# Kernel tuning notes

Measured on AMD Instinct MI355X. Metric: run time of the kernel, lower is better.

## Reference

```python
import jax, jax.numpy as jnp
import numpy as np

N = 32768       # total nodes = NUM_GRAPHS * T
F_IN = 32       # num_features
HC = 64         # hidden_channels
HEADS = 4
E = 524288      # edges before self-loops
NUM_GRAPHS = 64 # == batch.max()+1 by construction
T = 512         # time steps per graph (N // NUM_GRAPHS)
OUT = 24        # output_size
NEG_SLOPE = 0.2 # PyG GATConv default


def gat_layer(x, src, dst, W, a_src, a_dst, b, n_nodes):
    """PyG GATConv (concat=True) with edge softmax over incoming edges."""
    H, C = a_src.shape
    h = (x @ W).reshape(n_nodes, H, C)                    # [N,H,C]
    alpha_src = jnp.sum(h * a_src, axis=-1)               # [N,H]
    alpha_dst = jnp.sum(h * a_dst, axis=-1)               # [N,H]
    e = jax.nn.leaky_relu(alpha_src[src] + alpha_dst[dst], NEG_SLOPE)  # [E,H]
    m = jax.ops.segment_max(e, dst, num_segments=n_nodes)
    e = jnp.exp(e - m[dst])
    s = jax.ops.segment_sum(e, dst, num_segments=n_nodes)
    alpha = e / (s[dst] + 1e-16)                          # [E,H]
    msg = h[src] * alpha[..., None]                       # [E,H,C]
    out = jax.ops.segment_sum(msg, dst, num_segments=n_nodes)  # [N,H,C]
    return out.reshape(n_nodes, H * C) + b


def gru_layer(x, Wih, Whh, bih, bhh):
    """torch nn.GRU single layer, batch_first input x: [B,T,Hin] -> ([B,T,H], h_T)."""
    Bsz = x.shape[0]
    H = Whh.shape[1]

    def step(h, xt):
        gi = xt @ Wih.T + bih
        gh = h @ Whh.T + bhh
        ir, iz, inn = jnp.split(gi, 3, axis=-1)
        hr, hz, hn = jnp.split(gh, 3, axis=-1)
        r = jax.nn.sigmoid(ir + hr)
        z = jax.nn.sigmoid(iz + hz)
        n = jnp.tanh(inn + r * hn)
        h_new = (1.0 - z) * n + z * h
        return h_new, h_new

    h0 = jnp.zeros((Bsz, H), x.dtype)
    hT, ys = jax.lax.scan(step, h0, jnp.swapaxes(x, 0, 1))
    return jnp.swapaxes(ys, 0, 1), hT


def setup_inputs() -> dict:
    key = jax.random.key(0)
    ks = jax.random.split(key, 24)
    sc = 0.1
    inp = {
        "x": jax.random.normal(ks[0], (N, F_IN), dtype=jnp.float32),
        "edge_index": jax.random.randint(ks[1], (2, E), 0, N, dtype=jnp.int32),
        "batch": jnp.repeat(jnp.arange(NUM_GRAPHS, dtype=jnp.int32), T),
        # GAT layer 1: F_IN -> HC x HEADS (concat)
        "W1": sc * jax.random.normal(ks[2], (F_IN, HEADS * HC), dtype=jnp.float32),
        "a_src1": sc * jax.random.normal(ks[3], (HEADS, HC), dtype=jnp.float32),
        "a_dst1": sc * jax.random.normal(ks[4], (HEADS, HC), dtype=jnp.float32),
        "b1": jnp.zeros((HEADS * HC,), dtype=jnp.float32),
        # GAT layer 2: HEADS*HC -> HC, 1 head
        "W2": sc * jax.random.normal(ks[5], (HEADS * HC, HC), dtype=jnp.float32),
        "a_src2": sc * jax.random.normal(ks[6], (1, HC), dtype=jnp.float32),
        "a_dst2": sc * jax.random.normal(ks[7], (1, HC), dtype=jnp.float32),
        "b2": jnp.zeros((HC,), dtype=jnp.float32),
        # GRU (2 layers, input_size == hidden_size == HC)
        "gru_Wih0": sc * jax.random.normal(ks[8], (3 * HC, HC), dtype=jnp.float32),
        "gru_Whh0": sc * jax.random.normal(ks[9], (3 * HC, HC), dtype=jnp.float32),
        "gru_bih0": jnp.zeros((3 * HC,), dtype=jnp.float32),
        "gru_bhh0": jnp.zeros((3 * HC,), dtype=jnp.float32),
        "gru_Wih1": sc * jax.random.normal(ks[10], (3 * HC, HC), dtype=jnp.float32),
        "gru_Whh1": sc * jax.random.normal(ks[11], (3 * HC, HC), dtype=jnp.float32),
        "gru_bih1": jnp.zeros((3 * HC,), dtype=jnp.float32),
        "gru_bhh1": jnp.zeros((3 * HC,), dtype=jnp.float32),
        # Linear head
        "Wl": sc * jax.random.normal(ks[12], (OUT, HC), dtype=jnp.float32),
        "bl": jnp.zeros((OUT,), dtype=jnp.float32),
    }
    return inp


def reference(x, edge_index, batch, W1, a_src1, a_dst1, b1, W2, a_src2, a_dst2, b2,
              gru_Wih0, gru_Whh0, gru_bih0, gru_bhh0,
              gru_Wih1, gru_Whh1, gru_bih1, gru_bhh1, Wl, bl):
    # PyG GATConv default add_self_loops=True
    loops = jnp.arange(N, dtype=edge_index.dtype)
    src = jnp.concatenate([edge_index[0], loops])
    dst = jnp.concatenate([edge_index[1], loops])

    h = jax.nn.elu(gat_layer(x, src, dst, W1, a_src1, a_dst1, b1, N))   # [N, HEADS*HC]
    h = jax.nn.elu(gat_layer(h, src, dst, W2, a_src2, a_dst2, b2, N))   # [N, HC]

    # batch is repeat(arange(NUM_GRAPHS), T) so batch.max()+1 == NUM_GRAPHS (static)
    seq = h.reshape(NUM_GRAPHS, T, HC)
    seq, _ = gru_layer(seq, gru_Wih0, gru_Whh0, gru_bih0, gru_bhh0)
    _, hT = gru_layer(seq, gru_Wih1, gru_Whh1, gru_bih1, gru_bhh1)      # [B, HC]
    return hT @ Wl.T + bl                                               # [B, OUT]
```

## Files before the change

### kernel.cpp

```cpp
#include <hip/hip_runtime.h>
#include <hip/hip_bf16.h>

#define N_NODES 32768
#define F_IN    32
#define HC      64
#define HEADS   4
#define NE      524288
#define NET     (NE + N_NODES)
#define NG      64
#define TT      512
#define OUTF    24

__device__ __forceinline__ float lrelu(float x){ return x > 0.f ? x : 0.2f*x; }
__device__ __forceinline__ float eluf (float x){ return x > 0.f ? x : __expf(x)-1.f; }
__device__ __forceinline__ float sigmf(float x){ return 1.f/(1.f+__expf(-x)); }
__device__ __forceinline__ float tanhfast(float x){ return 1.f - 2.f/(__expf(2.f*x)+1.f); }
__device__ __forceinline__ float bcast(float v, int k){
  return __int_as_float(__builtin_amdgcn_readlane(__float_as_int(v), k));
}

__global__ __launch_bounds__(256) void k_deg(const int* __restrict__ ei,
                                             int* __restrict__ deg){
  int e = blockIdx.x*256 + threadIdx.x;
  int d = (e < NE) ? ei[NE+e] : (e - NE);
  atomicAdd(deg + d, 1);
}

__global__ __launch_bounds__(1024) void k_scan(const int* __restrict__ deg,
                                               int* __restrict__ rowptr){
  __shared__ int ps[1024];
  const int t = threadIdx.x;
  const int base = t*32;
  int local[32]; int s = 0;
  #pragma unroll
  for(int i=0;i<32;i++){ local[i]=deg[base+i]; s+=local[i]; }
  ps[t]=s; __syncthreads();
  for(int off=1; off<1024; off<<=1){
    int v = (t>=off) ? ps[t-off] : 0;
    __syncthreads();
    ps[t]+=v;
    __syncthreads();
  }
  int run = (t==0) ? 0 : ps[t-1];
  #pragma unroll
  for(int i=0;i<32;i++){ rowptr[base+i]=run; run+=local[i]; }
  if(t==1023) rowptr[N_NODES]=run;
}

__global__ __launch_bounds__(256) void k_fill(const int* __restrict__ ei,
                                              const int* __restrict__ rowptr,
                                              int* __restrict__ cur,
                                              int* __restrict__ col){
  int e = blockIdx.x*256 + threadIdx.x;
  int s, d;
  if(e < NE){ s = ei[e]; d = ei[NE+e]; } else { s = e-NE; d = s; }
  int pos = atomicAdd(cur + d, 1);
  col[rowptr[d] + pos] = s;
}

__global__ __launch_bounds__(256) void k_gemm1(const float* __restrict__ x,
                                               const float* __restrict__ W1,
                                               float* __restrict__ h1){
  __shared__ __align__(16) float xs[64*32];
  __shared__ __align__(16) float ws[32*256];
  const int tid = threadIdx.x;
  const int row0 = blockIdx.x*64;
  const float4* xg = (const float4*)(x + row0*F_IN);
  float4* xs4 = (float4*)xs;
  for(int i=tid;i<512;i+=256) xs4[i]=xg[i];
  const float4* wg=(const float4*)W1; float4* ws4=(float4*)ws;
  for(int i=tid;i<2048;i+=256) ws4[i]=wg[i];
  __syncthreads();
  float wc[32];
  #pragma unroll
  for(int k=0;k<32;k++) wc[k]=ws[k*256+tid];
  for(int r=0;r<64;r++){
    const float4* xr=(const float4*)(xs + r*32);
    float acc=0.f;
    #pragma unroll
    for(int k4=0;k4<8;k4++){
      float4 v=xr[k4];
      acc += v.x*wc[4*k4]+v.y*wc[4*k4+1]+v.z*wc[4*k4+2]+v.w*wc[4*k4+3];
    }
    h1[(row0+r)*256+tid]=acc;
  }
}

__global__ __launch_bounds__(256) void k_alpha1(const float* __restrict__ h1,
                                                const float* __restrict__ a_src,
                                                const float* __restrict__ a_dst,
                                                float* __restrict__ as1,
                                                float* __restrict__ ad1){
  int t = blockIdx.x*256 + threadIdx.x;
  int n = t>>2, h = t&3;
  const float4* hp=(const float4*)(h1 + n*256 + h*64);
  const float4* ap=(const float4*)(a_src + h*64);
  const float4* dp=(const float4*)(a_dst + h*64);
  float sa=0.f, sd=0.f;
  #pragma unroll
  for(int i=0;i<16;i++){
    float4 v=hp[i], a=ap[i], d=dp[i];
    sa += v.x*a.x+v.y*a.y+v.z*a.z+v.w*a.w;
    sd += v.x*d.x+v.y*d.y+v.z*d.z+v.w*d.w;
  }
  as1[t]=sa; ad1[t]=sd;
}

__global__ __launch_bounds__(256) void k_gat1(const int* __restrict__ rowptr,
                                              const int* __restrict__ col,
                                              const float* __restrict__ as1,
                                              const float* __restrict__ ad1,
                                              const float* __restrict__ h1,
                                              const float* __restrict__ b1,
                                              float* __restrict__ out1){
  const int node = blockIdx.x*4 + (threadIdx.x>>6);
  const int lane = threadIdx.x & 63;
  const int h    = lane>>4;
  const int beg = rowptr[node], end = rowptr[node+1];
  const float ad = ad1[node*4+h];
  float4 acc = make_float4(0.f,0.f,0.f,0.f);
  float s = 0.f;
  int j = beg;
  for(; j+1 < end; j += 2){
    int s0 = col[j], s1 = col[j+1];
    float w0 = __expf(lrelu(as1[s0*4+h] + ad));
    float w1 = __expf(lrelu(as1[s1*4+h] + ad));
    float4 v0 = *(const float4*)(h1 + s0*256 + lane*4);
    float4 v1 = *(const float4*)(h1 + s1*256 + lane*4);
    acc.x += w0*v0.x + w1*v1.x;
    acc.y += w0*v0.y + w1*v1.y;
    acc.z += w0*v0.z + w1*v1.z;
    acc.w += w0*v0.w + w1*v1.w;
    s += w0 + w1;
  }
  if(j < end){
    int s0 = col[j];
    float w0 = __expf(lrelu(as1[s0*4+h] + ad));
    float4 v0 = *(const float4*)(h1 + s0*256 + lane*4);
    acc.x += w0*v0.x; acc.y += w0*v0.y; acc.z += w0*v0.z; acc.w += w0*v0.w;
    s += w0;
  }
  const float inv = 1.f/(s + 1e-16f);
  float4 bb = ((const float4*)b1)[lane];
  float4 o;
  o.x = eluf(acc.x*inv + bb.x);
  o.y = eluf(acc.y*inv + bb.y);
  o.z = eluf(acc.z*inv + bb.z);
  o.w = eluf(acc.w*inv + bb.w);
  ((float4*)(out1 + node*256))[lane] = o;
}

__global__ __launch_bounds__(256) void k_gemm2(const float* __restrict__ in,
                                               const float* __restrict__ W2,
                                               float* __restrict__ h2){
  __shared__ __align__(16) float xs[64*256];
  const int tid=threadIdx.x;
  const int row0=blockIdx.x*64;
  const float4* xg=(const float4*)(in + row0*256);
  float4* xs4=(float4*)xs;
  for(int i=tid;i<4096;i+=256) xs4[i]=xg[i];
  __syncthreads();
  const int c0=(tid&15)*4;
  const int r0=(tid>>4)*4;
  float acc[4][4]={};
  for(int k=0;k<256;k+=4){
    float wv[4][4];
    #pragma unroll
    for(int i=0;i<4;i++){
      float4 w=*(const float4*)(W2+(k+i)*64+c0);
      wv[i][0]=w.x; wv[i][1]=w.y; wv[i][2]=w.z; wv[i][3]=w.w;
    }
    #pragma unroll
    for(int i=0;i<4;i++){
      float4 xv=*(const float4*)(xs+(r0+i)*256+k);
      #pragma unroll
      for(int j=0;j<4;j++)
        acc[i][j]+=xv.x*wv[0][j]+xv.y*wv[1][j]+xv.z*wv[2][j]+xv.w*wv[3][j];
    }
  }
  #pragma unroll
  for(int i=0;i<4;i++)
    *(float4*)(h2+(row0+r0+i)*64+c0)=make_float4(acc[i][0],acc[i][1],acc[i][2],acc[i][3]);
}

__global__ __launch_bounds__(256) void k_alpha2(const float* __restrict__ h2,
                                                const float* __restrict__ a_src,
                                                const float* __restrict__ a_dst,
                                                float* __restrict__ as2,
                                                float* __restrict__ ad2){
  int n = blockIdx.x*256 + threadIdx.x;
  const float4* hp=(const float4*)(h2+n*64);
  float sa=0.f, sd=0.f;
  #pragma unroll
  for(int i=0;i<16;i++){
    float4 v=hp[i];
    float4 a=((const float4*)a_src)[i];
    float4 d=((const float4*)a_dst)[i];
    sa+=v.x*a.x+v.y*a.y+v.z*a.z+v.w*a.w;
    sd+=v.x*d.x+v.y*d.y+v.z*d.z+v.w*d.w;
  }
  as2[n]=sa; ad2[n]=sd;
}

__global__ __launch_bounds__(256) void k_gat2(const int* __restrict__ rowptr,
                                              const int* __restrict__ col,
                                              const float* __restrict__ as2,
                                              const float* __restrict__ ad2,
                                              const float* __restrict__ h2,
                                              const float* __restrict__ b2,
                                              float* __restrict__ out2){
  const int node = blockIdx.x*4 + (threadIdx.x>>6);
  const int lane = threadIdx.x & 63;
  const int beg = rowptr[node], end = rowptr[node+1];
  const float ad = ad2[node];
  float acc = 0.f, s = 0.f;
  int j = beg;
  for(; j+1 < end; j += 2){
    int s0 = col[j], s1 = col[j+1];
    float w0 = __expf(lrelu(as2[s0] + ad));
    float w1 = __expf(lrelu(as2[s1] + ad));
    acc += w0*h2[s0*64+lane] + w1*h2[s1*64+lane];
    s += w0 + w1;
  }
  if(j < end){
    int s0 = col[j];
    float w0 = __expf(lrelu(as2[s0] + ad));
    acc += w0*h2[s0*64+lane];
    s += w0;
  }
  const float inv = 1.f/(s + 1e-16f);
  out2[node*64+lane] = eluf(acc*inv + b2[lane]);
}

__global__ __launch_bounds__(256) void k_gemm_gi(const float* __restrict__ in,
                                                 const float* __restrict__ Wih,
                                                 const float* __restrict__ bih,
                                                 float* __restrict__ gi){
  __shared__ __align__(16) float xs[64*64];
  __shared__ float wT[64*192];
  const int tid=threadIdx.x;
  const int row0=blockIdx.x*64;
  const float4* xg=(const float4*)(in+row0*64);
  float4* xs4=(float4*)xs;
  for(int i=tid;i<1024;i+=256) xs4[i]=xg[i];
  for(int i=tid;i<12288;i+=256){ wT[(i&63)*192+(i>>6)] = Wih[i]; }
  __syncthreads();
  if(tid<192){
    float wr[64];
    #pragma unroll
    for(int k=0;k<64;k++) wr[k]=wT[k*192+tid];
    const float bj=bih[tid];
    for(int r=0;r<64;r++){
      float acc=bj;
      const float4* xr=(const float4*)(xs+r*64);
      #pragma unroll
      for(int k4=0;k4<16;k4++){
        float4 v=xr[k4];
        acc+=v.x*wr[4*k4]+v.y*wr[4*k4+1]+v.z*wr[4*k4+2]+v.w*wr[4*k4+3];
      }
      gi[(row0+r)*192+tid]=acc;
    }
  }
}

__global__ __launch_bounds__(576,3) void k_gruR(const float* __restrict__ gi1,
                                                const float* __restrict__ Whh0,
                                                const float* __restrict__ bhh0,
                                                const float* __restrict__ Wih1,
                                                const float* __restrict__ bih1,
                                                const float* __restrict__ Whh1,
                                                const float* __restrict__ bhh1,
                                                const float* __restrict__ Wl,
                                                const float* __restrict__ bl,
                                                float* __restrict__ fout){
  __shared__ float h1s[64];
  __shared__ float h2s[64];
  __shared__ float gh1s[192];
  __shared__ float gi2s[192];
  __shared__ float gh2s[192];
  __shared__ float g1r[2][192];
  const int tid  = threadIdx.x;
  const int w    = tid >> 6;
  const int lane = tid & 63;
  const int b    = blockIdx.x;
  const float* gib = gi1 + (size_t)b*TT*192;

  const int crew = w/3;
  const int row  = (w%3)*64 + lane;
  const float* W  = (crew==0) ? Whh0 : (crew==1) ? Wih1 : Whh1;
  const float* bb = (crew==0) ? bhh0 : (crew==1) ? bih1 : bhh1;
  float* dst      = (crew==0) ? gh1s : (crew==1) ? gi2s : gh2s;

  const float4* wp = (const float4*)(W + row*64);
  float4 Wv0=wp[0],  Wv1=wp[1],  Wv2=wp[2],  Wv3=wp[3];
  float4 Wv4=wp[4],  Wv5=wp[5],  Wv6=wp[6],  Wv7=wp[7];
  float4 Wv8=wp[8],  Wv9=wp[9],  WvA=wp[10], WvB=wp[11];
  float4 WvC=wp[12], WvD=wp[13], WvE=wp[14], WvF=wp[15];
  const float bias = bb[row];

  float giv = 0.f;
  if(w < 3){
    g1r[0][row] = gib[row];
    giv = gib[192 + row];
  }
  if(tid < 64){ h1s[tid]=0.f; h2s[tid]=0.f; }
  __syncthreads();

  for(int i=0;i<=TT;i++){
    float hv = (crew==2) ? h2s[lane] : h1s[lane];
    if(w < 3){
      int pst = i+1;
      if(pst < TT) g1r[pst&1][row] = giv;
      int nst = i+2;
      if(nst < TT) giv = gib[nst*192 + row];
    }
    float a0=bias, a1=0.f, a2=0.f, a3=0.f;
#define DOT4(WV, BASE) \
    a0 = fmaf(bcast(hv, BASE+0), WV.x, a0); \
    a1 = fmaf(bcast(hv, BASE+1), WV.y, a1); \
    a2 = fmaf(bcast(hv, BASE+2), WV.z, a2); \
    a3 = fmaf(bcast(hv, BASE+3), WV.w, a3);
    DOT4(Wv0, 0)  DOT4(Wv1, 4)  DOT4(Wv2, 8)  DOT4(Wv3, 12)
    DOT4(Wv4, 16) DOT4(Wv5, 20) DOT4(Wv6, 24) DOT4(Wv7, 28)
    DOT4(Wv8, 32) DOT4(Wv9, 36) DOT4(WvA, 40) DOT4(WvB, 44)
    DOT4(WvC, 48) DOT4(WvD, 52) DOT4(WvE, 56) DOT4(WvF, 60)
#undef DOT4
    dst[row] = (a0+a1)+(a2+a3);
    __syncthreads();
    if(w == 0){
      if(i < TT){
        float r = sigmf(g1r[i&1][lane]     + gh1s[lane]);
        float z = sigmf(g1r[i&1][64+lane]  + gh1s[64+lane]);
        float n = tanhfast(g1r[i&1][128+lane] + r*gh1s[128+lane]);
        h1s[lane] = (1.f-z)*n + z*h1s[lane];
      }
    } else if(w == 3){
      if(i >= 1){
        float r = sigmf(gi2s[lane]     + gh2s[lane]);
        float z = sigmf(gi2s[64+lane]  + gh2s[64+lane]);
        float n = tanhfast(gi2s[128+lane] + r*gh2s[128+lane]);
        h2s[lane] = (1.f-z)*n + z*h2s[lane];
      }
    }
    __syncthreads();
  }

  if(tid < 24){
    float acc = bl[tid];
    const float4* wl4 = (const float4*)(Wl + tid*64);
    #pragma unroll
    for(int k4=0;k4<16;k4++){
      float4 h4 = *(const float4*)(h2s + 4*k4);
      float4 w4 = wl4[k4];
      acc += h4.x*w4.x + h4.y*w4.y + h4.z*w4.z + h4.w*w4.w;
    }
    fout[b*24+tid] = acc;
  }
}

extern "C" void kernel_launch(void* const* d_in, const int* in_sizes, int n_in,
                              void* d_out, int out_size, void* d_ws, size_t ws_size,
                              hipStream_t stream){
  const float* x     =(const float*)d_in[0];
  const int*   ei    =(const int*  )d_in[1];
  const float* W1    =(const float*)d_in[3];
  const float* a_src1=(const float*)d_in[4];
  const float* a_dst1=(const float*)d_in[5];
  const float* b1    =(const float*)d_in[6];
  const float* W2    =(const float*)d_in[7];
  const float* a_src2=(const float*)d_in[8];
  const float* a_dst2=(const float*)d_in[9];
  const float* b2    =(const float*)d_in[10];
  const float* Wih0  =(const float*)d_in[11];
  const float* Whh0  =(const float*)d_in[12];
  const float* bih0  =(const float*)d_in[13];
  const float* bhh0  =(const float*)d_in[14];
  const float* Wih1  =(const float*)d_in[15];
  const float* Whh1  =(const float*)d_in[16];
  const float* bih1  =(const float*)d_in[17];
  const float* bhh1  =(const float*)d_in[18];
  const float* Wl    =(const float*)d_in[19];
  const float* bl    =(const float*)d_in[20];

  float* ws   = (float*)d_ws;
  float* h1   = ws;
  float* gi   = ws;
  float* out1 = ws + 8388608;
  float* out2 = out1;
  float* h2   = ws + 16777216;
  float* as1  = ws + 18874368;
  float* ad1  = as1 + 131072;
  float* as2  = ad1 + 131072;
  float* ad2  = as2 + 32768;
  int* rowptr = (int*)(ad2 + 32768);
  int* deg    = rowptr + 32800;
  int* cur    = deg + 32768;
  int* col    = cur + 32768;
  float* fo   = (float*)d_out;

  hipMemsetAsync(deg, 0, 2*32768*sizeof(int), stream);

  k_deg  <<<2176,256,0,stream>>>(ei,deg);
  k_scan <<<1  ,1024,0,stream>>>(deg,rowptr);
  k_fill <<<2176,256,0,stream>>>(ei,rowptr,cur,col);

  k_gemm1 <<<512 ,256,0,stream>>>(x,W1,h1);
  k_alpha1<<<512 ,256,0,stream>>>(h1,a_src1,a_dst1,as1,ad1);
  k_gat1  <<<8192,256,0,stream>>>(rowptr,col,as1,ad1,h1,b1,out1);
  k_gemm2 <<<512 ,256,0,stream>>>(out1,W2,h2);
  k_alpha2<<<128 ,256,0,stream>>>(h2,a_src2,a_dst2,as2,ad2);
  k_gat2  <<<8192,256,0,stream>>>(rowptr,col,as2,ad2,h2,b2,out2);
  k_gemm_gi<<<512,256,0,stream>>>(out2,Wih0,bih0,gi);
  k_gruR  <<<64 ,576,0,stream>>>(gi,Whh0,bhh0,Wih1,bih1,Whh1,bhh1,Wl,bl,fo);
  (void)in_sizes; (void)n_in; (void)out_size; (void)ws_size;
}
```

Measured before the change: 819.4 us.

## Stage GRU input gates in 64-step LDS chunks instead of per-step prefetch

The recurrent GRU kernel now bulk-loads 64 timesteps of precomputed layer-0 input gates (48KB) into shared memory with float4 copies once per chunk. This replaces the per-step register prefetch and double-buffered LDS writes, taking the global load latency off the serial critical path. Weight registers are pinned with empty asm so they stay in VGPRs, and the launch-bounds occupancy hint drops to 1. In exchange, each chunk boundary adds a bulk-load stall plus a barrier, and the kernel uses much more LDS.

```diff
diff --git a/kernel.cpp b/kernel.cpp
--- a/kernel.cpp
+++ b/kernel.cpp
@@ -263,7 +263,7 @@
   }
 }
 
-__global__ __launch_bounds__(576,3) void k_gruR(const float* __restrict__ gi1,
+__global__ __launch_bounds__(576,1) void k_gruC(const float* __restrict__ gi1,
                                                 const float* __restrict__ Whh0,
                                                 const float* __restrict__ bhh0,
                                                 const float* __restrict__ Wih1,
@@ -278,7 +278,7 @@
   __shared__ float gh1s[192];
   __shared__ float gi2s[192];
   __shared__ float gh2s[192];
-  __shared__ float g1r[2][192];
+  __shared__ __align__(16) float gic[64*192];
   const int tid  = threadIdx.x;
   const int w    = tid >> 6;
   const int lane = tid & 63;
@@ -296,54 +296,68 @@
   float4 Wv4=wp[4],  Wv5=wp[5],  Wv6=wp[6],  Wv7=wp[7];
   float4 Wv8=wp[8],  Wv9=wp[9],  WvA=wp[10], WvB=wp[11];
   float4 WvC=wp[12], WvD=wp[13], WvE=wp[14], WvF=wp[15];
+#define PIN4(V) asm volatile("" : "+v"(V.x), "+v"(V.y), "+v"(V.z), "+v"(V.w))
+  PIN4(Wv0); PIN4(Wv1); PIN4(Wv2); PIN4(Wv3);
+  PIN4(Wv4); PIN4(Wv5); PIN4(Wv6); PIN4(Wv7);
+  PIN4(Wv8); PIN4(Wv9); PIN4(WvA); PIN4(WvB);
+  PIN4(WvC); PIN4(WvD); PIN4(WvE); PIN4(WvF);
+#undef PIN4
   const float bias = bb[row];
 
-  float giv = 0.f;
-  if(w < 3){
-    g1r[0][row] = gib[row];
-    giv = gib[192 + row];
-  }
   if(tid < 64){ h1s[tid]=0.f; h2s[tid]=0.f; }
   __syncthreads();
 
-  for(int i=0;i<=TT;i++){
-    float hv = (crew==2) ? h2s[lane] : h1s[lane];
-    if(w < 3){
-      int pst = i+1;
-      if(pst < TT) g1r[pst&1][row] = giv;
-      int nst = i+2;
-      if(nst < TT) giv = gib[nst*192 + row];
-    }
-    float a0=bias, a1=0.f, a2=0.f, a3=0.f;
 #define DOT4(WV, BASE) \
     a0 = fmaf(bcast(hv, BASE+0), WV.x, a0); \
     a1 = fmaf(bcast(hv, BASE+1), WV.y, a1); \
     a2 = fmaf(bcast(hv, BASE+2), WV.z, a2); \
     a3 = fmaf(bcast(hv, BASE+3), WV.w, a3);
-    DOT4(Wv0, 0)  DOT4(Wv1, 4)  DOT4(Wv2, 8)  DOT4(Wv3, 12)
-    DOT4(Wv4, 16) DOT4(Wv5, 20) DOT4(Wv6, 24) DOT4(Wv7, 28)
-    DOT4(Wv8, 32) DOT4(Wv9, 36) DOT4(WvA, 40) DOT4(WvB, 44)
-    DOT4(WvC, 48) DOT4(WvD, 52) DOT4(WvE, 56) DOT4(WvF, 60)
+#define MATVEC() do{ \
+    float hv = (crew==2) ? h2s[lane] : h1s[lane]; \
+    float a0=bias, a1=0.f, a2=0.f, a3=0.f; \
+    DOT4(Wv0, 0)  DOT4(Wv1, 4)  DOT4(Wv2, 8)  DOT4(Wv3, 12) \
+    DOT4(Wv4, 16) DOT4(Wv5, 20) DOT4(Wv6, 24) DOT4(Wv7, 28) \
+    DOT4(Wv8, 32) DOT4(Wv9, 36) DOT4(WvA, 40) DOT4(WvB, 44) \
+    DOT4(WvC, 48) DOT4(WvD, 52) DOT4(WvE, 56) DOT4(WvF, 60) \
+    dst[row] = (a0+a1)+(a2+a3); \
+  }while(0)
+
+  for(int c=0;c<8;c++){
+    const float4* g4 = (const float4*)gib + (size_t)c*3072;
+    float4* gic4 = (float4*)gic;
+    for(int l=tid; l<3072; l+=576) gic4[l] = g4[l];
+    __syncthreads();
+    for(int j=0;j<64;j++){
+      const int i = c*64 + j;
+      MATVEC();
+      __syncthreads();
+      if(w == 0){
+        float r = sigmf(gic[j*192+lane]     + gh1s[lane]);
+        float z = sigmf(gic[j*192+64+lane]  + gh1s[64+lane]);
+        float n = tanhfast(gic[j*192+128+lane] + r*gh1s[128+lane]);
+        h1s[lane] = (1.f-z)*n + z*h1s[lane];
+      } else if(w == 3){
+        if(i >= 1){
+          float r = sigmf(gi2s[lane]     + gh2s[lane]);
+          float z = sigmf(gi2s[64+lane]  + gh2s[64+lane]);
+          float n = tanhfast(gi2s[128+lane] + r*gh2s[128+lane]);
+          h2s[lane] = (1.f-z)*n + z*h2s[lane];
+        }
+      }
+      __syncthreads();
+    }
+  }
+  MATVEC();
+  __syncthreads();
+  if(w == 3){
+    float r = sigmf(gi2s[lane]     + gh2s[lane]);
+    float z = sigmf(gi2s[64+lane]  + gh2s[64+lane]);
+    float n = tanhfast(gi2s[128+lane] + r*gh2s[128+lane]);
+    h2s[lane] = (1.f-z)*n + z*h2s[lane];
+  }
+  __syncthreads();
+#undef MATVEC
 #undef DOT4
-    dst[row] = (a0+a1)+(a2+a3);
-    __syncthreads();
-    if(w == 0){
-      if(i < TT){
-        float r = sigmf(g1r[i&1][lane]     + gh1s[lane]);
-        float z = sigmf(g1r[i&1][64+lane]  + gh1s[64+lane]);
-        float n = tanhfast(g1r[i&1][128+lane] + r*gh1s[128+lane]);
-        h1s[lane] = (1.f-z)*n + z*h1s[lane];
-      }
-    } else if(w == 3){
-      if(i >= 1){
-        float r = sigmf(gi2s[lane]     + gh2s[lane]);
-        float z = sigmf(gi2s[64+lane]  + gh2s[64+lane]);
-        float n = tanhfast(gi2s[128+lane] + r*gh2s[128+lane]);
-        h2s[lane] = (1.f-z)*n + z*h2s[lane];
-      }
-    }
-    __syncthreads();
-  }
 
   if(tid < 24){
     float acc = bl[tid];
@@ -411,6 +425,6 @@
   k_alpha2<<<128 ,256,0,stream>>>(h2,a_src2,a_dst2,as2,ad2);
   k_gat2  <<<8192,256,0,stream>>>(rowptr,col,as2,ad2,h2,b2,out2);
   k_gemm_gi<<<512,256,0,stream>>>(out2,Wih0,bih0,gi);
-  k_gruR  <<<64 ,576,0,stream>>>(gi,Whh0,bhh0,Wih1,bih1,Whh1,bhh1,Wl,bl,fo);
+  k_gruC  <<<64 ,576,0,stream>>>(gi,Whh0,bhh0,Wih1,bih1,Whh1,bhh1,Wl,bl,fo);
   (void)in_sizes; (void)n_in; (void)out_size; (void)ws_size;
 }
```

Measured after the change: 833.7 us. About the same (+1.7%).

## Reorder GAT layer 1 to aggregate raw features before the linear projection

Applied to the files above, without the earlier changes.

Uses linearity to reorder GAT layer 1. Attention logits come from x times a precomputed W1·a vector. Neighbours are aggregated on raw 32-wide input features per head instead of 256-wide projected features, and the W1 projection, softmax normalisation, bias and ELU are applied afterwards in a fused GEMM epilogue. This shrinks the gather traffic in the edge aggregation from 1 KB per edge to 128 B per edge and removes the h1 intermediate. The cost is a small extra precompute kernel, a 128-wide agg buffer, and changed floating-point summation order.

```diff
diff --git a/kernel.cpp b/kernel.cpp
--- a/kernel.cpp
+++ b/kernel.cpp
@@ -58,96 +58,136 @@
   col[rowptr[d] + pos] = s;
 }
 
-__global__ __launch_bounds__(256) void k_gemm1(const float* __restrict__ x,
-                                               const float* __restrict__ W1,
-                                               float* __restrict__ h1){
-  __shared__ __align__(16) float xs[64*32];
-  __shared__ __align__(16) float ws[32*256];
+__global__ __launch_bounds__(256) void k_prep(const float* __restrict__ W1,
+                                              const float* __restrict__ a_src,
+                                              const float* __restrict__ a_dst,
+                                              float* __restrict__ p){
+  const int t = threadIdx.x;
+  const int k = t>>3, q = t&7;
+  const int h = q>>1, isd = q&1;
+  const float* av = (isd ? a_dst : a_src) + h*64;
+  const float* wr = W1 + k*256 + h*64;
+  float acc = 0.f;
+  #pragma unroll
+  for(int c=0;c<64;c++) acc += wr[c]*av[c];
+  p[(isd?128:0) + k*4 + h] = acc;
+}
+
+__global__ __launch_bounds__(256) void k_alpha1x(const float* __restrict__ x,
+                                                 const float* __restrict__ p,
+                                                 float* __restrict__ as1,
+                                                 float* __restrict__ ad1){
+  __shared__ float ps[256];
+  const int tid = threadIdx.x;
+  ps[tid] = p[tid];
+  __syncthreads();
+  const int n = blockIdx.x*256 + tid;
+  const float4* xr = (const float4*)(x + n*32);
+  float sa0=0.f,sa1=0.f,sa2=0.f,sa3=0.f, sd0=0.f,sd1=0.f,sd2=0.f,sd3=0.f;
+  #pragma unroll
+  for(int k4=0;k4<8;k4++){
+    float4 v = xr[k4];
+    const float* pa = ps + (4*k4)*4;
+    const float* pd = ps + 128 + (4*k4)*4;
+    sa0 += v.x*pa[0] + v.y*pa[4] + v.z*pa[8]  + v.w*pa[12];
+    sa1 += v.x*pa[1] + v.y*pa[5] + v.z*pa[9]  + v.w*pa[13];
+    sa2 += v.x*pa[2] + v.y*pa[6] + v.z*pa[10] + v.w*pa[14];
+    sa3 += v.x*pa[3] + v.y*pa[7] + v.z*pa[11] + v.w*pa[15];
+    sd0 += v.x*pd[0] + v.y*pd[4] + v.z*pd[8]  + v.w*pd[12];
+    sd1 += v.x*pd[1] + v.y*pd[5] + v.z*pd[9]  + v.w*pd[13];
+    sd2 += v.x*pd[2] + v.y*pd[6] + v.z*pd[10] + v.w*pd[14];
+    sd3 += v.x*pd[3] + v.y*pd[7] + v.z*pd[11] + v.w*pd[15];
+  }
+  *(float4*)(as1+n*4) = make_float4(sa0,sa1,sa2,sa3);
+  *(float4*)(ad1+n*4) = make_float4(sd0,sd1,sd2,sd3);
+}
+
+__global__ __launch_bounds__(256) void k_gatx(const int* __restrict__ rowptr,
+                                              const int* __restrict__ col,
+                                              const float* __restrict__ as1,
+                                              const float* __restrict__ ad1,
+                                              const float* __restrict__ x,
+                                              float* __restrict__ agg,
+                                              float* __restrict__ s14){
+  const int node = blockIdx.x*4 + (threadIdx.x>>6);
+  const int lane = threadIdx.x & 63;
+  const int h0   = lane>>5;
+  const int c    = lane & 31;
+  const int beg = rowptr[node], end = rowptr[node+1];
+  const float adA = ad1[node*4 + h0];
+  const float adB = ad1[node*4 + h0 + 2];
+  float accA=0.f, accB=0.f, wsA=0.f, wsB=0.f;
+  int j = beg;
+  for(; j+1 < end; j += 2){
+    int s0 = col[j], s1 = col[j+1];
+    float4 q0 = *(const float4*)(as1 + s0*4);
+    float4 q1 = *(const float4*)(as1 + s1*4);
+    float aA0 = h0 ? q0.y : q0.x, aB0 = h0 ? q0.w : q0.z;
+    float aA1 = h0 ? q1.y : q1.x, aB1 = h0 ? q1.w : q1.z;
+    float wA0 = __expf(lrelu(aA0 + adA));
+    float wB0 = __expf(lrelu(aB0 + adB));
+    float wA1 = __expf(lrelu(aA1 + adA));
+    float wB1 = __expf(lrelu(aB1 + adB));
+    float x0 = x[s0*32 + c];
+    float x1 = x[s1*32 + c];
+    accA += wA0*x0 + wA1*x1;
+    accB += wB0*x0 + wB1*x1;
+    wsA  += wA0 + wA1;
+    wsB  += wB0 + wB1;
+  }
+  if(j < end){
+    int s0 = col[j];
+    float4 q0 = *(const float4*)(as1 + s0*4);
+    float aA0 = h0 ? q0.y : q0.x, aB0 = h0 ? q0.w : q0.z;
+    float wA0 = __expf(lrelu(aA0 + adA));
+    float wB0 = __expf(lrelu(aB0 + adB));
+    float x0 = x[s0*32 + c];
+    accA += wA0*x0; accB += wB0*x0;
+    wsA += wA0; wsB += wB0;
+  }
+  agg[node*128 + h0*32 + c]     = accA;
+  agg[node*128 + (h0+2)*32 + c] = accB;
+  if(c == 0){
+    s14[node*4 + h0]     = wsA;
+    s14[node*4 + h0 + 2] = wsB;
+  }
+}
+
+__global__ __launch_bounds__(256) void k_gemm1e(const float* __restrict__ agg,
+                                                const float* __restrict__ W1,
+                                                const float* __restrict__ s14,
+                                                const float* __restrict__ b1,
+                                                float* __restrict__ out1){
+  __shared__ __align__(16) float ags[64*128];
+  __shared__ __align__(16) float wsh[32*256];
+  __shared__ float sv[64*4];
   const int tid = threadIdx.x;
   const int row0 = blockIdx.x*64;
-  const float4* xg = (const float4*)(x + row0*F_IN);
-  float4* xs4 = (float4*)xs;
-  for(int i=tid;i<512;i+=256) xs4[i]=xg[i];
-  const float4* wg=(const float4*)W1; float4* ws4=(float4*)ws;
+  const float4* ag = (const float4*)(agg + row0*128);
+  float4* ags4 = (float4*)ags;
+  for(int i=tid;i<2048;i+=256) ags4[i]=ag[i];
+  const float4* wg=(const float4*)W1; float4* ws4=(float4*)wsh;
   for(int i=tid;i<2048;i+=256) ws4[i]=wg[i];
+  const float4* sg=(const float4*)(s14 + row0*4);
+  float4* sv4=(float4*)sv;
+  if(tid<64) sv4[tid]=sg[tid];
   __syncthreads();
+  const int h = tid>>6;
   float wc[32];
   #pragma unroll
-  for(int k=0;k<32;k++) wc[k]=ws[k*256+tid];
+  for(int k=0;k<32;k++) wc[k]=wsh[k*256 + tid];
+  const float bb = b1[tid];
   for(int r=0;r<64;r++){
-    const float4* xr=(const float4*)(xs + r*32);
+    const float4* ar=(const float4*)(ags + r*128 + h*32);
     float acc=0.f;
     #pragma unroll
     for(int k4=0;k4<8;k4++){
-      float4 v=xr[k4];
+      float4 v=ar[k4];
       acc += v.x*wc[4*k4]+v.y*wc[4*k4+1]+v.z*wc[4*k4+2]+v.w*wc[4*k4+3];
     }
-    h1[(row0+r)*256+tid]=acc;
-  }
-}
-
-__global__ __launch_bounds__(256) void k_alpha1(const float* __restrict__ h1,
-                                                const float* __restrict__ a_src,
-                                                const float* __restrict__ a_dst,
-                                                float* __restrict__ as1,
-                                                float* __restrict__ ad1){
-  int t = blockIdx.x*256 + threadIdx.x;
-  int n = t>>2, h = t&3;
-  const float4* hp=(const float4*)(h1 + n*256 + h*64);
-  const float4* ap=(const float4*)(a_src + h*64);
-  const float4* dp=(const float4*)(a_dst + h*64);
-  float sa=0.f, sd=0.f;
-  #pragma unroll
-  for(int i=0;i<16;i++){
-    float4 v=hp[i], a=ap[i], d=dp[i];
-    sa += v.x*a.x+v.y*a.y+v.z*a.z+v.w*a.w;
-    sd += v.x*d.x+v.y*d.y+v.z*d.z+v.w*d.w;
-  }
-  as1[t]=sa; ad1[t]=sd;
-}
-
-__global__ __launch_bounds__(256) void k_gat1(const int* __restrict__ rowptr,
-                                              const int* __restrict__ col,
-                                              const float* __restrict__ as1,
-                                              const float* __restrict__ ad1,
-                                              const float* __restrict__ h1,
-                                              const float* __restrict__ b1,
-                                              float* __restrict__ out1){
-  const int node = blockIdx.x*4 + (threadIdx.x>>6);
-  const int lane = threadIdx.x & 63;
-  const int h    = lane>>4;
-  const int beg = rowptr[node], end = rowptr[node+1];
-  const float ad = ad1[node*4+h];
-  float4 acc = make_float4(0.f,0.f,0.f,0.f);
-  float s = 0.f;
-  int j = beg;
-  for(; j+1 < end; j += 2){
-    int s0 = col[j], s1 = col[j+1];
-    float w0 = __expf(lrelu(as1[s0*4+h] + ad));
-    float w1 = __expf(lrelu(as1[s1*4+h] + ad));
-    float4 v0 = *(const float4*)(h1 + s0*256 + lane*4);
-    float4 v1 = *(const float4*)(h1 + s1*256 + lane*4);
-    acc.x += w0*v0.x + w1*v1.x;
-    acc.y += w0*v0.y + w1*v1.y;
-    acc.z += w0*v0.z + w1*v1.z;
-    acc.w += w0*v0.w + w1*v1.w;
-    s += w0 + w1;
-  }
-  if(j < end){
-    int s0 = col[j];
-    float w0 = __expf(lrelu(as1[s0*4+h] + ad));
-    float4 v0 = *(const float4*)(h1 + s0*256 + lane*4);
-    acc.x += w0*v0.x; acc.y += w0*v0.y; acc.z += w0*v0.z; acc.w += w0*v0.w;
-    s += w0;
-  }
-  const float inv = 1.f/(s + 1e-16f);
-  float4 bb = ((const float4*)b1)[lane];
-  float4 o;
-  o.x = eluf(acc.x*inv + bb.x);
-  o.y = eluf(acc.y*inv + bb.y);
-  o.z = eluf(acc.z*inv + bb.z);
-  o.w = eluf(acc.w*inv + bb.w);
-  ((float4*)(out1 + node*256))[lane] = o;
+    float inv = 1.f/(sv[r*4+h] + 1e-16f);
+    out1[(row0+r)*256 + tid] = eluf(acc*inv + bb);
+  }
 }
 
 __global__ __launch_bounds__(256) void k_gemm2(const float* __restrict__ in,
@@ -383,7 +423,8 @@
   const float* bl    =(const float*)d_in[20];
 
   float* ws   = (float*)d_ws;
-  float* h1   = ws;
+  float* agg  = ws;
+  float* s14  = ws + 4194304;
   float* gi   = ws;
   float* out1 = ws + 8388608;
   float* out2 = out1;
@@ -392,7 +433,8 @@
   float* ad1  = as1 + 131072;
   float* as2  = ad1 + 131072;
   float* ad2  = as2 + 32768;
-  int* rowptr = (int*)(ad2 + 32768);
+  float* pbuf = ad2 + 32768;
+  int* rowptr = (int*)(pbuf + 512);
   int* deg    = rowptr + 32800;
   int* cur    = deg + 32768;
   int* col    = cur + 32768;
@@ -400,17 +442,18 @@
 
   hipMemsetAsync(deg, 0, 2*32768*sizeof(int), stream);
 
-  k_deg  <<<2176,256,0,stream>>>(ei,deg);
-  k_scan <<<1  ,1024,0,stream>>>(deg,rowptr);
-  k_fill <<<2176,256,0,stream>>>(ei,rowptr,cur,col);
-
-  k_gemm1 <<<512 ,256,0,stream>>>(x,W1,h1);
-  k_alpha1<<<512 ,256,0,stream>>>(h1,a_src1,a_dst1,as1,ad1);
-  k_gat1  <<<8192,256,0,stream>>>(rowptr,col,as1,ad1,h1,b1,out1);
-  k_gemm2 <<<512 ,256,0,stream>>>(out1,W2,h2);
-  k_alpha2<<<128 ,256,0,stream>>>(h2,a_src2,a_dst2,as2,ad2);
-  k_gat2  <<<8192,256,0,stream>>>(rowptr,col,as2,ad2,h2,b2,out2);
-  k_gemm_gi<<<512,256,0,stream>>>(out2,Wih0,bih0,gi);
-  k_gruR  <<<64 ,576,0,stream>>>(gi,Whh0,bhh0,Wih1,bih1,Whh1,bhh1,Wl,bl,fo);
+  k_deg   <<<2176,256,0,stream>>>(ei,deg);
+  k_scan  <<<1  ,1024,0,stream>>>(deg,rowptr);
+  k_fill  <<<2176,256,0,stream>>>(ei,rowptr,cur,col);
+
+  k_prep   <<<1   ,256,0,stream>>>(W1,a_src1,a_dst1,pbuf);
+  k_alpha1x<<<128 ,256,0,stream>>>(x,pbuf,as1,ad1);
+  k_gatx   <<<8192,256,0,stream>>>(rowptr,col,as1,ad1,x,agg,s14);
+  k_gemm1e <<<512 ,256,0,stream>>>(agg,W1,s14,b1,out1);
+  k_gemm2  <<<512 ,256,0,stream>>>(out1,W2,h2);
+  k_alpha2 <<<128 ,256,0,stream>>>(h2,a_src2,a_dst2,as2,ad2);
+  k_gat2   <<<8192,256,0,stream>>>(rowptr,col,as2,ad2,h2,b2,out2);
+  k_gemm_gi<<<512 ,256,0,stream>>>(out2,Wih0,bih0,gi);
+  k_gruR   <<<64  ,576,0,stream>>>(gi,Whh0,bhh0,Wih1,bih1,Whh1,bhh1,Wl,bl,fo);
   (void)in_sizes; (void)n_in; (void)out_size; (void)ws_size;
 }
```

Result: faster. 779.9 us (-4.8%).
